# Kernel tuning notes

Measured on AMD Instinct MI355X. Metric: run time of the kernel, lower is better.

Reference implementation:

```python
import jax, jax.numpy as jnp
import numpy as np

B, S, D_IN, D_OUT, H = 4, 2048, 1024, 1024, 16
HD = D_OUT // H  # head_dim = 64


def setup_inputs() -> dict:
    key = jax.random.key(0)
    ks = jax.random.split(key, 9)
    sc_in = 1.0 / np.sqrt(D_IN)
    sc_out = 1.0 / np.sqrt(D_OUT)
    return {
        "x": jax.random.normal(ks[0], (B, S, D_IN), dtype=jnp.float32),
        "Wq": jax.random.normal(ks[1], (D_IN, D_OUT), dtype=jnp.float32) * sc_in,
        "bq": jax.random.normal(ks[2], (D_OUT,), dtype=jnp.float32) * 0.01,
        "Wk": jax.random.normal(ks[3], (D_IN, D_OUT), dtype=jnp.float32) * sc_in,
        "bk": jax.random.normal(ks[4], (D_OUT,), dtype=jnp.float32) * 0.01,
        "Wv": jax.random.normal(ks[5], (D_IN, D_OUT), dtype=jnp.float32) * sc_in,
        "bv": jax.random.normal(ks[6], (D_OUT,), dtype=jnp.float32) * 0.01,
        "Wo": jax.random.normal(ks[7], (D_OUT, D_OUT), dtype=jnp.float32) * sc_out,
        "bo": jax.random.normal(ks[8], (D_OUT,), dtype=jnp.float32) * 0.01,
    }


def reference(x, Wq, bq, Wk, bk, Wv, bv, Wo, bo):
    b, s, _ = x.shape
    # QKV projections -> [b, h, s, hd]
    def proj(W, bias):
        return (x @ W + bias).reshape(b, s, H, HD).transpose(0, 2, 1, 3)
    q, k, v = proj(Wq, bq), proj(Wk, bk), proj(Wv, bv)
    # scaled scores [b, h, s, s] with causal mask (future positions -> -inf)
    scores = jnp.einsum("bhqd,bhkd->bhqk", q, k) / jnp.sqrt(jnp.float32(HD))
    causal = jnp.triu(jnp.ones((s, s), dtype=bool), k=1)
    scores = jnp.where(causal, -jnp.inf, scores)
    attn = jax.nn.softmax(scores, axis=-1)  # dropout p=0.0 -> identity
    ctx = jnp.einsum("bhqk,bhkd->bhqd", attn, v)
    ctx = ctx.transpose(0, 2, 1, 3).reshape(b, s, D_OUT)
    return ctx @ Wo + bo
```

## Files before the change

kernel.cpp:

```cpp
#include <hip/hip_runtime.h>
#include <hip/hip_bf16.h>

#define B_   4
#define S_   2048
#define H_   16
#define HD_  64
#define D_   1024
#define M_   (B_ * S_)
#define N3_  3072

typedef unsigned short u16;
typedef __bf16 bf16x8 __attribute__((ext_vector_type(8)));
typedef float  f32x4  __attribute__((ext_vector_type(4)));
typedef int    i32x4  __attribute__((ext_vector_type(4)));
typedef unsigned short u16x8 __attribute__((ext_vector_type(8)));
typedef unsigned short u16x4 __attribute__((ext_vector_type(4)));

__device__ __forceinline__ float b2f(u16 u) {
    unsigned int x = ((unsigned int)u) << 16;
    return __builtin_bit_cast(float, x);
}
__device__ __forceinline__ u16 f2b(float f) {
    unsigned int x = __builtin_bit_cast(unsigned int, f);
    x += 0x7fffu + ((x >> 16) & 1u);
    return (u16)(x >> 16);
}

typedef const __attribute__((address_space(1))) unsigned int* gas_u32p;
typedef __attribute__((address_space(3))) unsigned int* las_u32p;
__device__ __forceinline__ void gl_lds16(const u16* g, u16* lds_base) {
    __builtin_amdgcn_global_load_lds((gas_u32p)g, (las_u32p)lds_base, 16, 0, 0);
}

__global__ __launch_bounds__(256) void cvt_k(const float* __restrict__ in,
                                             u16* __restrict__ out) {
    size_t i = ((size_t)blockIdx.x * 256 + threadIdx.x) * 8;
    float4 a = *(const float4*)(in + i);
    float4 b = *(const float4*)(in + i + 4);
    *(u16x8*)(out + i) = u16x8{f2b(a.x), f2b(a.y), f2b(a.z), f2b(a.w),
                               f2b(b.x), f2b(b.y), f2b(b.z), f2b(b.w)};
}

__global__ __launch_bounds__(256) void transpose4_k(
    const float* __restrict__ w0, const float* __restrict__ w1,
    const float* __restrict__ w2, const float* __restrict__ w3,
    u16* __restrict__ oqkv, u16* __restrict__ owo, float scale0) {
    __shared__ u16 t[32][33];
    const int z = blockIdx.z;
    const float* in = (z == 0) ? w0 : (z == 1) ? w1 : (z == 2) ? w2 : w3;
    u16* out = (z < 3) ? oqkv + (size_t)z * D_ * D_ : owo;
    const float sc = (z == 0) ? scale0 : 1.0f;
    const int x0 = blockIdx.x * 32, y0 = blockIdx.y * 32;
    const int tx = threadIdx.x & 31, ty = threadIdx.x >> 5;
#pragma unroll
    for (int i = 0; i < 32; i += 8)
        t[ty + i][tx] = f2b(in[(size_t)(y0 + ty + i) * D_ + x0 + tx] * sc);
    __syncthreads();
#pragma unroll
    for (int i = 0; i < 32; i += 8)
        out[(size_t)(x0 + ty + i) * D_ + y0 + tx] = t[tx][ty + i];
}

#define BM 128
#define BN 128
#define BK 64

template <int MODE>
__global__ __launch_bounds__(256) void gemm_core(
    const u16* __restrict__ A, const u16* __restrict__ Bt,
    const float* __restrict__ b0, const float* __restrict__ b1,
    const float* __restrict__ b2, float cscale,
    void* __restrict__ O0, void* __restrict__ O1, void* __restrict__ O2,
    int M, int N, int K)
{
    __shared__ __align__(16) u16 As[BM * BK];
    __shared__ __align__(16) u16 Bs[BN * BK];

    const int tid  = threadIdx.x;
    const int lane = tid & 63;
    const int wave = tid >> 6;
    const int wr = wave >> 1, wc = wave & 1;
    const int l15 = lane & 15, quad = lane >> 4;
    const int m0 = blockIdx.x * BM, n0 = blockIdx.y * BN;
    const int r8 = lane >> 3;
    const int csw = ((lane & 7) ^ r8) * 8;

    f32x4 acc[4][4] = {};

    for (int k0 = 0; k0 < K; k0 += BK) {
#pragma unroll
        for (int i = 0; i < 4; ++i) {
            const int row = wave * 32 + i * 8 + r8;
            gl_lds16(A  + (size_t)(m0 + row) * K + k0 + csw,
                     As + (wave * 32 + i * 8) * BK);
            gl_lds16(Bt + (size_t)(n0 + row) * K + k0 + csw,
                     Bs + (wave * 32 + i * 8) * BK);
        }
        __syncthreads();
        bf16x8 af[4][2], bfr[4][2];
#pragma unroll
        for (int t = 0; t < 4; ++t) {
            const u16* ap = As + (wr * 64 + t * 16 + l15) * BK;
            const u16* bp = Bs + (wc * 64 + t * 16 + l15) * BK;
            const int s7 = l15 & 7;
            af[t][0]  = *(const bf16x8*)(ap + ((quad    ) ^ s7) * 8);
            af[t][1]  = *(const bf16x8*)(ap + ((quad + 4) ^ s7) * 8);
            bfr[t][0] = *(const bf16x8*)(bp + ((quad    ) ^ s7) * 8);
            bfr[t][1] = *(const bf16x8*)(bp + ((quad + 4) ^ s7) * 8);
        }
#pragma unroll
        for (int mt = 0; mt < 4; ++mt)
#pragma unroll
            for (int nt = 0; nt < 4; ++nt) {
                acc[mt][nt] = __builtin_amdgcn_mfma_f32_16x16x32_bf16(
                    af[mt][0], bfr[nt][0], acc[mt][nt], 0, 0, 0);
                acc[mt][nt] = __builtin_amdgcn_mfma_f32_16x16x32_bf16(
                    af[mt][1], bfr[nt][1], acc[mt][nt], 0, 0, 0);
            }
        __syncthreads();
    }

#pragma unroll
    for (int nt = 0; nt < 4; ++nt) {
        const int col = n0 + wc * 64 + nt * 16 + l15;
        if constexpr (MODE == 1) {
            const float bv = b0[col];
#pragma unroll
            for (int mt = 0; mt < 4; ++mt) {
                const int rbase = m0 + wr * 64 + mt * 16 + quad * 4;
#pragma unroll
                for (int r2 = 0; r2 < 4; ++r2)
                    ((float*)O0)[(size_t)(rbase + r2) * N + col] =
                        acc[mt][nt][r2] + bv;
            }
        } else {
            const int qidx = col >> 10, ncol = col & (D_ - 1);
            const float bv = (qidx == 0) ? b0[ncol] * cscale
                           : (qidx == 1) ? b1[ncol] : b2[ncol];
#pragma unroll
            for (int mt = 0; mt < 4; ++mt) {
                const int rbase = m0 + wr * 64 + mt * 16 + quad * 4;
                if (qidx == 2) {
                    const int bidx = rbase >> 11, s = rbase & (S_ - 1);
                    const int hh = ncol >> 6, hd = ncol & 63;
                    u16x4 pk{f2b(acc[mt][nt][0] + bv), f2b(acc[mt][nt][1] + bv),
                             f2b(acc[mt][nt][2] + bv), f2b(acc[mt][nt][3] + bv)};
                    *(u16x4*)((u16*)O2 +
                        (((size_t)(bidx * H_ + hh)) * HD_ + hd) * S_ + s) = pk;
                } else {
                    u16* dst = (qidx == 0) ? (u16*)O0 : (u16*)O1;
#pragma unroll
                    for (int r2 = 0; r2 < 4; ++r2)
                        dst[(size_t)(rbase + r2) * D_ + ncol] =
                            f2b(acc[mt][nt][r2] + bv);
                }
            }
        }
    }
}

__global__ __launch_bounds__(256, 4) void attn_mfma_k(
    const u16* __restrict__ Qm, const u16* __restrict__ Km,
    const u16* __restrict__ Vtg, u16* __restrict__ Om)
{
    __shared__ __align__(16) u16 Kbuf[2][64 * 64];
    __shared__ __align__(16) u16 Vbuf[2][64 * 64];
    __shared__ __align__(16) u16 Ps[4][16 * 64];

    const int tid  = threadIdx.x;
    const int lane = tid & 63;
    const int wave = tid >> 6;
    const int l15  = lane & 15;
    const int quad = lane >> 4;
    const int s7   = l15 & 7;
    const int bh = blockIdx.x, b = bh >> 4, h = bh & (H_ - 1);
    const int j  = blockIdx.y;
    const int dg0 = j, dg1 = 31 - j;

    const u16* Qg = Qm + (size_t)b * S_ * D_ + h * HD_;
    const u16* Kg = Km + (size_t)b * S_ * D_ + h * HD_;
    const u16* Vg = Vtg + ((size_t)(b * H_ + h)) * HD_ * S_;

    bf16x8 qf0[2], qf1[2];
    {
        const u16* qp = Qg + (size_t)(dg0 * 64 + wave * 16 + l15) * D_ + quad * 8;
        qf0[0] = *(const bf16x8*)qp; qf0[1] = *(const bf16x8*)(qp + 32);
        qp = Qg + (size_t)(dg1 * 64 + wave * 16 + l15) * D_ + quad * 8;
        qf1[0] = *(const bf16x8*)qp; qf1[1] = *(const bf16x8*)(qp + 32);
    }

    f32x4 of0[4] = {}, of1[4] = {};
    float lacc0 = 0.f, lacc1 = 0.f;
    const int qloc = wave * 16 + l15;
    const int r8 = lane >> 3;
    const int csw = ((lane & 7) ^ r8) * 8;
    const int srcA = l15 + ((quad & 1) << 5);
    const int srcB = srcA + 16;

    auto stage = [&](int t, int bsel) {
        u16* kb = Kbuf[bsel];
        u16* vb = Vbuf[bsel];
#pragma unroll
        for (int i = 0; i < 2; ++i) {
            const int row = wave * 16 + i * 8 + r8;
            gl_lds16(Kg + (size_t)(t * 64 + row) * D_ + csw,
                     kb + (wave * 16 + i * 8) * 64);
            gl_lds16(Vg + (size_t)row * S_ + t * 64 + csw,
                     vb + (wave * 16 + i * 8) * 64);
        }
    };

    auto pass = [&](const bf16x8 (&q)[2], f32x4 (&o)[4], float& la,
                    bool domask, const u16* kb, const u16* vb) {
        f32x4 sf[4];
#pragma unroll
        for (int kt = 0; kt < 4; ++kt) {
            const u16* kp = kb + (kt * 16 + l15) * 64;
            bf16x8 k0 = *(const bf16x8*)(kp + ((quad    ) ^ s7) * 8);
            bf16x8 k1 = *(const bf16x8*)(kp + ((quad + 4) ^ s7) * 8);
            f32x4 a = {};
            a = __builtin_amdgcn_mfma_f32_16x16x32_bf16(k0, q[0], a, 0, 0, 0);
            a = __builtin_amdgcn_mfma_f32_16x16x32_bf16(k1, q[1], a, 0, 0, 0);
            sf[kt] = a;
        }
        unsigned int w[4][2];
        float ls = 0.f;
        if (domask) {
#pragma unroll
            for (int kt = 0; kt < 4; ++kt)
#pragma unroll
                for (int hh = 0; hh < 2; ++hh) {
                    float v0 = sf[kt][2 * hh], v1 = sf[kt][2 * hh + 1];
                    if (kt * 16 + quad * 4 + 2 * hh     > qloc) v0 = -INFINITY;
                    if (kt * 16 + quad * 4 + 2 * hh + 1 > qloc) v1 = -INFINITY;
                    float p0 = __builtin_amdgcn_exp2f(v0);
                    float p1 = __builtin_amdgcn_exp2f(v1);
                    ls += p0 + p1;
                    w[kt][hh] = (__builtin_bit_cast(unsigned int, p0) >> 16) |
                                (__builtin_bit_cast(unsigned int, p1) & 0xFFFF0000u);
                }
        } else {
#pragma unroll
            for (int kt = 0; kt < 4; ++kt)
#pragma unroll
                for (int hh = 0; hh < 2; ++hh) {
                    float p0 = __builtin_amdgcn_exp2f(sf[kt][2 * hh]);
                    float p1 = __builtin_amdgcn_exp2f(sf[kt][2 * hh + 1]);
                    ls += p0 + p1;
                    w[kt][hh] = (__builtin_bit_cast(unsigned int, p0) >> 16) |
                                (__builtin_bit_cast(unsigned int, p1) & 0xFFFF0000u);
                }
        }
        la += ls;
        const bool hi = (quad & 2) != 0;
        i32x4 f0, f1;
        {
            int a0, a1;
            a0 = __shfl((int)w[0][0], srcA); a1 = __shfl((int)w[1][0], srcA);
            f0.x = hi ? a1 : a0;
            a0 = __shfl((int)w[0][1], srcA); a1 = __shfl((int)w[1][1], srcA);
            f0.y = hi ? a1 : a0;
            a0 = __shfl((int)w[0][0], srcB); a1 = __shfl((int)w[1][0], srcB);
            f0.z = hi ? a1 : a0;
            a0 = __shfl((int)w[0][1], srcB); a1 = __shfl((int)w[1][1], srcB);
            f0.w = hi ? a1 : a0;
            a0 = __shfl((int)w[2][0], srcA); a1 = __shfl((int)w[3][0], srcA);
            f1.x = hi ? a1 : a0;
            a0 = __shfl((int)w[2][1], srcA); a1 = __shfl((int)w[3][1], srcA);
            f1.y = hi ? a1 : a0;
            a0 = __shfl((int)w[2][0], srcB); a1 = __shfl((int)w[3][0], srcB);
            f1.z = hi ? a1 : a0;
            a0 = __shfl((int)w[2][1], srcB); a1 = __shfl((int)w[3][1], srcB);
            f1.w = hi ? a1 : a0;
        }
        bf16x8 pf0 = __builtin_bit_cast(bf16x8, f0);
        bf16x8 pf1 = __builtin_bit_cast(bf16x8, f1);
#pragma unroll
        for (int dt = 0; dt < 4; ++dt) {
            const u16* vp = vb + (dt * 16 + l15) * 64;
            bf16x8 v0 = *(const bf16x8*)(vp + ((quad    ) ^ s7) * 8);
            bf16x8 v1 = *(const bf16x8*)(vp + ((quad + 4) ^ s7) * 8);
            o[dt] = __builtin_amdgcn_mfma_f32_16x16x32_bf16(v0, pf0, o[dt], 0, 0, 0);
            o[dt] = __builtin_amdgcn_mfma_f32_16x16x32_bf16(v1, pf1, o[dt], 0, 0, 0);
        }
    };

    const int T = 32 - j;
    stage(0, 0);
    for (int t = 0; t < T; ++t) {
        __syncthreads();
        if (t + 1 < T) stage(t + 1, (t + 1) & 1);
        const u16* kb = Kbuf[t & 1];
        const u16* vb = Vbuf[t & 1];
        if (t <= dg0) pass(qf0, of0, lacc0, t == dg0, kb, vb);
        pass(qf1, of1, lacc1, t == dg1, kb, vb);
    }

    u16* pw = Ps[wave];
    auto epi = [&](const f32x4 (&o)[4], float la, int dgq) {
        float ls = la;
        ls += __shfl_xor(ls, 16);
        ls += __shfl_xor(ls, 32);
        const float inv = 1.f / ls;
#pragma unroll
        for (int dt = 0; dt < 4; ++dt) {
            const int g = dt * 16 + quad * 4;
            const int pos = ((g >> 3) ^ s7) * 8 + (g & 7);
            *(u16x4*)(pw + l15 * 64 + pos) =
                u16x4{f2b(o[dt][0] * inv), f2b(o[dt][1] * inv),
                      f2b(o[dt][2] * inv), f2b(o[dt][3] * inv)};
        }
        const int r  = lane >> 2;
        const int cp = lane & 3;
        u16x8 o0 = *(const u16x8*)(pw + r * 64 + ((2 * cp    ) ^ (r & 7)) * 8);
        u16x8 o1 = *(const u16x8*)(pw + r * 64 + ((2 * cp + 1) ^ (r & 7)) * 8);
        u16* op = Om + ((size_t)(b * S_ + dgq * 64 + wave * 16 + r)) * D_ + h * 64 + cp * 16;
        *(u16x8*)op = o0;
        *(u16x8*)(op + 8) = o1;
    };
    epi(of0, lacc0, dg0);
    epi(of1, lacc1, dg1);
}

extern "C" void kernel_launch(void* const* d_in, const int* in_sizes, int n_in,
                              void* d_out, int out_size, void* d_ws, size_t ws_size,
                              hipStream_t stream)
{
    (void)in_sizes; (void)n_in; (void)out_size; (void)ws_size;
    const float* x  = (const float*)d_in[0];
    const float* Wq = (const float*)d_in[1];
    const float* bq = (const float*)d_in[2];
    const float* Wk = (const float*)d_in[3];
    const float* bk = (const float*)d_in[4];
    const float* Wv = (const float*)d_in[5];
    const float* bv = (const float*)d_in[6];
    const float* Wo = (const float*)d_in[7];
    const float* bo = (const float*)d_in[8];

    const float cscale = 0.18033688011112042f;

    u16* ws = (u16*)d_ws;
    const size_t MD = (size_t)M_ * D_;
    const size_t DD = (size_t)D_ * D_;
    u16* xb    = ws;
    u16* Qb    = xb + MD;
    u16* Kb    = Qb + MD;
    u16* Vtb   = Kb + MD;
    u16* Cb    = Vtb + MD;
    u16* WqkvT = Cb + MD;
    u16* WoT   = WqkvT + 3 * DD;

    cvt_k<<<M_ * D_ / 2048, 256, 0, stream>>>(x, xb);

    transpose4_k<<<dim3(D_ / 32, D_ / 32, 4), 256, 0, stream>>>(
        Wq, Wk, Wv, Wo, WqkvT, WoT, cscale);

    gemm_core<0><<<dim3(M_ / BM, N3_ / BN), 256, 0, stream>>>(
        xb, WqkvT, bq, bk, bv, cscale, Qb, Kb, Vtb, M_, N3_, D_);

    attn_mfma_k<<<dim3(B_ * H_, 16), 256, 0, stream>>>(Qb, Kb, Vtb, Cb);

    gemm_core<1><<<dim3(M_ / BM, D_ / BN), 256, 0, stream>>>(
        Cb, WoT, bo, nullptr, nullptr, 1.0f, d_out, nullptr, nullptr, M_, D_, D_);
}
```

Measured before the change: 273.4 us.

## Add 256x256 double-buffered QKV GEMM kernel with interleaved async LDS staging

Replaces the 128x128 QKV projection GEMM with a dedicated 256x256-tile kernel using 512 threads, double-buffered LDS, and direct global-to-LDS loads spread across the MFMA phases. The larger tile raises arithmetic intensity and cuts global traffic per FLOP, while the interleaved staging aims to hide load latency behind MFMAs. In exchange it uses 128KB of LDS and many accumulators per thread, which limits occupancy, and the grid is small (32x12 blocks), so wave quantization on the CUs is a risk.

```diff
diff --git a/kernel.cpp b/kernel.cpp
--- a/kernel.cpp
+++ b/kernel.cpp
@@ -59,6 +59,144 @@
 #pragma unroll
     for (int i = 0; i < 32; i += 8)
         out[(size_t)(x0 + ty + i) * D_ + y0 + tx] = t[tx][ty + i];
+}
+
+#define QBM 256
+#define QBN 256
+#define QBK 64
+
+__global__ __launch_bounds__(512, 2) void gemm_qkv256(
+    const u16* __restrict__ A, const u16* __restrict__ Bt,
+    const float* __restrict__ b0, const float* __restrict__ b1,
+    const float* __restrict__ b2, float cscale,
+    u16* __restrict__ Qo, u16* __restrict__ Ko, u16* __restrict__ Vto,
+    int M, int N, int K)
+{
+    __shared__ __align__(16) u16 As[2][QBM * QBK];
+    __shared__ __align__(16) u16 Bs[2][QBN * QBK];
+
+    const int tid  = threadIdx.x;
+    const int lane = tid & 63;
+    const int wave = tid >> 6;
+    const int wr = wave >> 2, wc = wave & 3;
+    const int l15 = lane & 15, quad = lane >> 4, s7 = l15 & 7;
+    const int r8  = lane >> 3;
+    const int csw = ((lane & 7) ^ r8) * 8;
+    const int m0 = blockIdx.x * QBM, n0 = blockIdx.y * QBN;
+    (void)M;
+
+    const u16* Ag = A  + (size_t)(m0 + wave * 8 + r8) * K + csw;
+    const u16* Bg = Bt + (size_t)(n0 + wave * 8 + r8) * K + csw;
+    u16* AsW = &As[0][0] + wave * 8 * QBK;
+    u16* BsW = &Bs[0][0] + wave * 8 * QBK;
+
+    auto stgA = [&](int buf, int half, int i, int kt) {
+        gl_lds16(Ag + (size_t)(half * 128 + i * 64) * K + kt * QBK,
+                 AsW + buf * (QBM * QBK) + (half * 128 + i * 64) * QBK);
+    };
+    auto stgB = [&](int buf, int half, int i, int kt) {
+        gl_lds16(Bg + (size_t)(half * 128 + i * 64) * K + kt * QBK,
+                 BsW + buf * (QBN * QBK) + (half * 128 + i * 64) * QBK);
+    };
+
+    f32x4 acc[8][4] = {};
+
+    stgA(0, 0, 0, 0); stgA(0, 0, 1, 0); stgA(0, 1, 0, 0); stgA(0, 1, 1, 0);
+    stgB(0, 0, 0, 0); stgB(0, 0, 1, 0); stgB(0, 1, 0, 0); stgB(0, 1, 1, 0);
+    stgB(1, 0, 0, 1); stgB(1, 0, 1, 1); stgB(1, 1, 0, 1); stgB(1, 1, 1, 1);
+    asm volatile("s_waitcnt vmcnt(4)" ::: "memory");
+    __builtin_amdgcn_s_barrier();
+
+    const int NIT = K / (2 * QBK);
+    for (int it = 0; it < NIT; ++it) {
+        const bool last = (it == NIT - 1);
+        const int t1 = 2 * it + 1, t2 = 2 * it + 2, t3 = 2 * it + 3;
+#pragma unroll
+        for (int hb = 0; hb < 2; ++hb) {
+            const u16* as = &As[hb][0];
+            const u16* bs = &Bs[hb][0];
+            bf16x8 bn[4][2];
+#pragma unroll
+            for (int q = 0; q < 4; ++q) {
+                if (q == 0) {
+#pragma unroll
+                    for (int n = 0; n < 4; ++n) {
+                        const u16* bp = bs + (wc * 64 + n * 16 + l15) * QBK;
+                        bn[n][0] = *(const bf16x8*)(bp + ((quad    ) ^ s7) * 8);
+                        bn[n][1] = *(const bf16x8*)(bp + ((quad + 4) ^ s7) * 8);
+                    }
+                }
+                bf16x8 af[2][2];
+#pragma unroll
+                for (int dm = 0; dm < 2; ++dm) {
+                    const u16* ap = as + (wr * 128 + (2 * q + dm) * 16 + l15) * QBK;
+                    af[dm][0] = *(const bf16x8*)(ap + ((quad    ) ^ s7) * 8);
+                    af[dm][1] = *(const bf16x8*)(ap + ((quad + 4) ^ s7) * 8);
+                }
+                const int p = hb * 4 + q;
+                if (!last) {
+                    if (p == 0) { stgA(1, 0, 0, t1); stgA(1, 0, 1, t1); }
+                    if (p == 1) { stgA(1, 1, 0, t1); stgA(1, 1, 1, t1); }
+                    if (p == 2) { stgB(0, 0, 0, t2); stgB(0, 0, 1, t2); }
+                    if (p == 3) { stgB(0, 1, 0, t2); stgB(0, 1, 1, t2); }
+                    if (p == 4) { stgA(0, 0, 0, t2); stgA(0, 0, 1, t2); }
+                    if (p == 5) { stgA(0, 1, 0, t2); stgA(0, 1, 1, t2); }
+                    if (p == 6) { stgB(1, 0, 0, t3); stgB(1, 0, 1, t3); }
+                    if (p == 7) { stgB(1, 1, 0, t3); stgB(1, 1, 1, t3); }
+                } else {
+                    if (p == 0) { stgA(1, 0, 0, t1); stgA(1, 0, 1, t1); }
+                    if (p == 1) { stgA(1, 1, 0, t1); stgA(1, 1, 1, t1); }
+                }
+                __builtin_amdgcn_s_barrier();
+                asm volatile("s_waitcnt lgkmcnt(0)" ::: "memory");
+                __builtin_amdgcn_sched_barrier(0);
+                __builtin_amdgcn_s_setprio(1);
+#pragma unroll
+                for (int dm = 0; dm < 2; ++dm)
+#pragma unroll
+                    for (int n = 0; n < 4; ++n) {
+                        acc[2 * q + dm][n] = __builtin_amdgcn_mfma_f32_16x16x32_bf16(
+                            af[dm][0], bn[n][0], acc[2 * q + dm][n], 0, 0, 0);
+                        acc[2 * q + dm][n] = __builtin_amdgcn_mfma_f32_16x16x32_bf16(
+                            af[dm][1], bn[n][1], acc[2 * q + dm][n], 0, 0, 0);
+                    }
+                __builtin_amdgcn_s_setprio(0);
+                if (q == 3) {
+                    if (!last)
+                        asm volatile("s_waitcnt vmcnt(4)" ::: "memory");
+                    else if (hb == 0)
+                        asm volatile("s_waitcnt vmcnt(0)" ::: "memory");
+                }
+                __builtin_amdgcn_s_barrier();
+            }
+        }
+    }
+
+#pragma unroll
+    for (int nt = 0; nt < 4; ++nt) {
+        const int col = n0 + wc * 64 + nt * 16 + l15;
+        const int qidx = col >> 10, ncol = col & (D_ - 1);
+        const float bv = (qidx == 0) ? b0[ncol] * cscale
+                       : (qidx == 1) ? b1[ncol] : b2[ncol];
+#pragma unroll
+        for (int mt = 0; mt < 8; ++mt) {
+            const int rbase = m0 + wr * 128 + mt * 16 + quad * 4;
+            if (qidx == 2) {
+                const int bidx = rbase >> 11, s = rbase & (S_ - 1);
+                const int hh = ncol >> 6, hd = ncol & 63;
+                u16x4 pk{f2b(acc[mt][nt][0] + bv), f2b(acc[mt][nt][1] + bv),
+                         f2b(acc[mt][nt][2] + bv), f2b(acc[mt][nt][3] + bv)};
+                *(u16x4*)(Vto +
+                    (((size_t)(bidx * H_ + hh)) * HD_ + hd) * S_ + s) = pk;
+            } else {
+                u16* dst = (qidx == 0) ? Qo : Ko;
+#pragma unroll
+                for (int r2 = 0; r2 < 4; ++r2)
+                    dst[(size_t)(rbase + r2) * D_ + ncol] =
+                        f2b(acc[mt][nt][r2] + bv);
+            }
+        }
+    }
 }
 
 #define BM 128
@@ -355,7 +493,7 @@
     transpose4_k<<<dim3(D_ / 32, D_ / 32, 4), 256, 0, stream>>>(
         Wq, Wk, Wv, Wo, WqkvT, WoT, cscale);
 
-    gemm_core<0><<<dim3(M_ / BM, N3_ / BN), 256, 0, stream>>>(
+    gemm_qkv256<<<dim3(M_ / QBM, N3_ / QBN), 512, 0, stream>>>(
         xb, WqkvT, bq, bk, bv, cscale, Qb, Kb, Vtb, M_, N3_, D_);
 
     attn_mfma_k<<<dim3(B_ * H_, 16), 256, 0, stream>>>(Qb, Kb, Vtb, Cb);
```

Result: no change. 270.0 us (-1.2%).
